# Kernel tuning notes

Hardware: AMD Instinct MI355X
Metric: run time of the kernel (lower is better)

Reference implementation:

```python
import jax, jax.numpy as jnp
import numpy as np

N = 100000

def _gcn_layer(x, W, b, row, col, n):
    # x: [N, Fin] -> lin -> [N, Fout]
    h = x @ W + b
    # degree over row (includes self loops), dtype follows x
    deg = jnp.zeros((n,), dtype=h.dtype).at[row].add(jnp.ones_like(row, dtype=h.dtype))
    dis = deg ** -0.5
    norm = dis[row] * dis[col]                      # [E]
    msg = norm[:, None] * h[row]                    # gather + scale: [E, Fout]
    return jax.ops.segment_sum(msg, col, num_segments=n)  # scatter-add at targets


def setup_inputs() -> dict:
    key = jax.random.key(0)
    ks = jax.random.split(key, 10)
    x = jax.random.normal(ks[0], (N, 32), dtype=jnp.float32)
    feat = jax.random.normal(ks[1], (N, 32), dtype=jnp.float32)
    edge_index = jax.random.randint(ks[2], (2, 1600000), 0, N, dtype=jnp.int64)
    # params (torch Linear stored as [in, out] here; y = x @ W + b)
    def lin(k, fin, fout):
        s = 1.0 / np.sqrt(fin)
        kw, kb = jax.random.split(k)
        W = jax.random.uniform(kw, (fin, fout), minval=-s, maxval=s, dtype=jnp.float32)
        b = jax.random.uniform(kb, (fout,), minval=-s, maxval=s, dtype=jnp.float32)
        return W, b
    W1, b1 = lin(ks[3], 64, 64)
    W2, b2 = lin(ks[4], 64, 64)
    Wfc, bfc = lin(ks[5], 64, 64)
    return {"x": x, "feat": feat, "edge_index": edge_index,
            "W1": W1, "b1": b1, "W2": W2, "b2": b2, "Wfc": Wfc, "bfc": bfc}


def reference(x, feat, edge_index, W1, b1, W2, b2, Wfc, bfc):
    n = x.shape[0]
    h = jnp.concatenate([x, feat], axis=-1)          # [N, 64]
    # add self loops once (same augmented edge set used by every layer)
    loops = jnp.arange(n, dtype=edge_index.dtype)
    row = jnp.concatenate([edge_index[0], loops])
    col = jnp.concatenate([edge_index[1], loops])
    h = jax.nn.relu(_gcn_layer(h, W1, b1, row, col, n))
    h = jax.nn.relu(_gcn_layer(h, W2, b2, row, col, n))
    return jax.nn.relu(h @ Wfc + bfc)                # [N, 64]
```

## Files before the change

### kernel.cpp

```cpp
#include <hip/hip_runtime.h>
#include <hip/hip_bf16.h>


#define FDIM 64
#define NPART 8
#define GPB 64
#define NB 256
#define BW 512
#define MAXP 1024
#define GPLIN 1024

typedef __hip_bfloat16 bf16;
typedef short v8s __attribute__((ext_vector_type(8)));
typedef float v4f __attribute__((ext_vector_type(4)));

__global__ void k_h(const int* __restrict__ row, const int* __restrict__ col,
                    unsigned* __restrict__ part, int* __restrict__ M,
                    int E, int n, int psize, int P, int CH) {
    __shared__ unsigned sm[12512];
    int t = threadIdx.x, b = blockIdx.x;
    if (b < NPART * GPB) {
        int p = b >> 6, g = b & 63;
        int base = p * psize;
        int lim = n - base; if (lim > psize) lim = psize;
        for (int i = t; i < lim; i += 256) sm[i] = 0u;
        __syncthreads();
        for (int e = g * 256 + t; e < E; e += GPB * 256) {
            int r = row[e] - base;
            if ((unsigned)r < (unsigned)lim) atomicAdd(&sm[r], 1u);
        }
        __syncthreads();
        unsigned* dst = part + ((size_t)p * GPB + g) * psize;
        for (int i = t; i < lim; i += 256) dst[i] = sm[i];
    } else {
        int cb = b - NPART * GPB;
        int* h = (int*)sm;
        for (int i = t; i < P; i += 256) h[i] = 0;
        __syncthreads();
        int s = cb * CH, e = min(s + CH, E);
        for (int i = s + t; i < e; i += 256)
            atomicAdd(&h[col[i] >> 9], 1);
        __syncthreads();
        for (int p = t; p < P; p += 256) M[p * NB + cb] = h[p];
    }
}

__global__ void k_ds1(const unsigned* __restrict__ part, float* __restrict__ dis,
                      int* __restrict__ M, int* __restrict__ bsum,
                      int n, int psize, int ndis, int P) {
    __shared__ int sc[256];
    int t = threadIdx.x, b = blockIdx.x;
    if (b < ndis) {
        int i = b * 256 + t;
        if (i >= n) return;
        int p = i / psize, loc = i - p * psize;
        const unsigned* src = part + (size_t)p * GPB * psize + loc;
        unsigned s = 0;
        #pragma unroll 8
        for (int g = 0; g < GPB; ++g) s += src[(size_t)g * psize];
        dis[i] = rsqrtf((float)s + 1.0f);
    } else {
        int sb = b - ndis;
        int i = sb * 256 + t;
        int v = M[i];
        sc[t] = v;
        __syncthreads();
        for (int d = 1; d < 256; d <<= 1) {
            int u = (t >= d) ? sc[t - d] : 0;
            __syncthreads(); sc[t] += u; __syncthreads();
        }
        M[i] = sc[t] - v;
        if (t == 255) bsum[sb] = sc[255];
    }
}

__global__ void k_csc(const int* __restrict__ row, const int* __restrict__ col,
                      const int* __restrict__ M, const int* __restrict__ bsum,
                      int* __restrict__ s4, int E, int CH, int P) {
    __shared__ int sc[256];
    __shared__ int bs[256];
    __shared__ int cur[MAXP];
    int t = threadIdx.x, b = blockIdx.x;
    int v = (t < P) ? bsum[t] : 0;
    sc[t] = v;
    __syncthreads();
    for (int d = 1; d < 256; d <<= 1) {
        int u = (t >= d) ? sc[t - d] : 0;
        __syncthreads(); sc[t] += u; __syncthreads();
    }
    bs[t] = sc[t] - v;
    __syncthreads();
    for (int p = t; p < P; p += 256) cur[p] = bs[p] + M[p * NB + b];
    __syncthreads();
    int s = b * CH, e = min(s + CH, E);
    for (int i = s + t; i < e; i += 256) {
        int r = row[i], c = col[i];
        int pos = atomicAdd(&cur[c >> 9], 1);
        s4[pos] = (r << 9) | (c & 511);
    }
}

__global__ __launch_bounds__(256, 4)
void k_fl(const int* __restrict__ s4, const int* __restrict__ M,
          const int* __restrict__ bsum, int* __restrict__ rows4,
          int* __restrict__ off,
          const float* __restrict__ x, const float* __restrict__ feat,
          const float* __restrict__ W, const float* __restrict__ bvec,
          const float* __restrict__ dis, bf16* __restrict__ g1,
          int n, int E, int P) {
    __shared__ int sc[256];
    __shared__ int bs[256];
    __shared__ int hist[BW];
    __shared__ int loff[BW];
    __shared__ int tmp[256];
    __shared__ float sIn[4][FDIM];
    int t = threadIdx.x, b = blockIdx.x;
    if (b < P) {
        int v = (t < P) ? bsum[t] : 0;
        sc[t] = v;
        __syncthreads();
        for (int d = 1; d < 256; d <<= 1) {
            int u = (t >= d) ? sc[t - d] : 0;
            __syncthreads(); sc[t] += u; __syncthreads();
        }
        bs[t] = sc[t] - v;
        __syncthreads();
        int gs = bs[b];
        int ge = gs + bsum[b];
        int c0 = b << 9;
        int lim = n - c0; if (lim > BW) lim = BW;
        hist[2 * t] = 0; hist[2 * t + 1] = 0;
        __syncthreads();
        for (int i = gs + t; i < ge; i += 256)
            atomicAdd(&hist[s4[i] & 511], 1);
        __syncthreads();
        int s0 = hist[2 * t], s1v = hist[2 * t + 1];
        int ps = s0 + s1v;
        tmp[t] = ps;
        __syncthreads();
        for (int d = 1; d < 256; d <<= 1) {
            int u = (t >= d) ? tmp[t - d] : 0;
            __syncthreads(); tmp[t] += u; __syncthreads();
        }
        int ex = tmp[t] - ps;
        loff[2 * t] = ex;
        loff[2 * t + 1] = ex + s0;
        __syncthreads();
        for (int i = t; i < lim; i += 256) off[c0 + i] = gs + loff[i];
        if (b == P - 1 && t == 0) off[n] = E;
        __syncthreads();
        for (int i = gs + t; i < ge; i += 256) {
            int v2 = s4[i];
            int pos = gs + atomicAdd(&loff[v2 & 511], 1);
            rows4[pos] = v2 >> 9;
        }
    } else {
        int local = t >> 6, j = t & 63;
        float Wreg[FDIM];
        #pragma unroll
        for (int k = 0; k < FDIM; ++k) Wreg[k] = W[k * FDIM + j];
        float bj = bvec[j];
        int gw = (b - P) * 4 + local;
        int nwl = GPLIN * 4;
        for (int w = gw; w < n; w += nwl) {
            sIn[local][j] = (j < 32) ? x[(size_t)w * 32 + j]
                                     : feat[(size_t)w * 32 + (j - 32)];
            __threadfence_block();
            float o = bj;
            #pragma unroll
            for (int k4 = 0; k4 < 16; ++k4) {
                float4 h4 = *(const float4*)&sIn[local][k4 * 4];
                o = fmaf(h4.x, Wreg[4 * k4 + 0], o);
                o = fmaf(h4.y, Wreg[4 * k4 + 1], o);
                o = fmaf(h4.z, Wreg[4 * k4 + 2], o);
                o = fmaf(h4.w, Wreg[4 * k4 + 3], o);
            }
            g1[(size_t)w * FDIM + j] = __float2bfloat16(dis[w] * o);
            __threadfence_block();
        }
    }
}

__global__ __launch_bounds__(256, 8)
void k_gather(const int* __restrict__ rows4, const int* __restrict__ off,
              const float* __restrict__ dis, const bf16* __restrict__ g,
              bf16* __restrict__ a, int n) {
    int t = blockIdx.x * blockDim.x + threadIdx.x;
    int w = t >> 6, j = t & 63;
    if (w >= n) return;
    float acc0 = __bfloat162float(g[(size_t)w * FDIM + j]);
    float acc1 = 0.0f;
    int k = off[w], e = off[w + 1];
    for (; k + 8 <= e; k += 8) {
        int r0 = rows4[k], r1 = rows4[k + 1], r2 = rows4[k + 2], r3 = rows4[k + 3];
        int r4 = rows4[k + 4], r5 = rows4[k + 5], r6 = rows4[k + 6], r7 = rows4[k + 7];
        float h0 = __bfloat162float(g[(size_t)r0 * FDIM + j]);
        float h1 = __bfloat162float(g[(size_t)r1 * FDIM + j]);
        float h2 = __bfloat162float(g[(size_t)r2 * FDIM + j]);
        float h3 = __bfloat162float(g[(size_t)r3 * FDIM + j]);
        float h4 = __bfloat162float(g[(size_t)r4 * FDIM + j]);
        float h5 = __bfloat162float(g[(size_t)r5 * FDIM + j]);
        float h6 = __bfloat162float(g[(size_t)r6 * FDIM + j]);
        float h7 = __bfloat162float(g[(size_t)r7 * FDIM + j]);
        acc0 += h0; acc1 += h1; acc0 += h2; acc1 += h3;
        acc0 += h4; acc1 += h5; acc0 += h6; acc1 += h7;
    }
    for (; k + 2 <= e; k += 2) {
        int r0 = rows4[k], r1 = rows4[k + 1];
        acc0 += __bfloat162float(g[(size_t)r0 * FDIM + j]);
        acc1 += __bfloat162float(g[(size_t)r1 * FDIM + j]);
    }
    if (k < e) acc0 += __bfloat162float(g[(size_t)rows4[k] * FDIM + j]);
    a[(size_t)w * FDIM + j] = __float2bfloat16(fmaxf(dis[w] * (acc0 + acc1), 0.0f));
}

template <bool FINAL>
__global__ __launch_bounds__(256, 4)
void k_mat(const bf16* __restrict__ A, const float* __restrict__ W,
           const float* __restrict__ bvec, const float* __restrict__ dis,
           void* __restrict__ outp, int n) {
    __shared__ __align__(16) bf16 sWt[FDIM * FDIM];
    int t = threadIdx.x;
    for (int idx = t; idx < FDIM * FDIM; idx += 256) {
        int kk = idx >> 6, nn = idx & 63;
        sWt[nn * FDIM + kk] = __float2bfloat16(W[idx]);
    }
    __syncthreads();
    int wave = t >> 6, lane = t & 63;
    int quad = lane >> 4, l15 = lane & 15;
    v8s bfr[4][2];
    #pragma unroll
    for (int nt = 0; nt < 4; ++nt) {
        #pragma unroll
        for (int kf = 0; kf < 2; ++kf)
            bfr[nt][kf] = *(const v8s*)&sWt[(nt * 16 + l15) * FDIM + kf * 32 + quad * 8];
    }
    float bj[4];
    #pragma unroll
    for (int nt = 0; nt < 4; ++nt) bj[nt] = bvec[nt * 16 + l15];

    int ntiles = (n + 15) >> 4;
    int step = gridDim.x * 4;
    for (int tile = blockIdx.x * 4 + wave; tile < ntiles; tile += step) {
        int m0 = tile << 4;
        int mA = m0 + l15; if (mA >= n) mA = n - 1;
        v8s af0 = *(const v8s*)&A[(size_t)mA * FDIM + quad * 8];
        v8s af1 = *(const v8s*)&A[(size_t)mA * FDIM + 32 + quad * 8];
        v4f acc[4];
        #pragma unroll
        for (int nt = 0; nt < 4; ++nt) {
            acc[nt] = (v4f){0.f, 0.f, 0.f, 0.f};
            acc[nt] = __builtin_amdgcn_mfma_f32_16x16x32_bf16(af0, bfr[nt][0], acc[nt], 0, 0, 0);
            acc[nt] = __builtin_amdgcn_mfma_f32_16x16x32_bf16(af1, bfr[nt][1], acc[nt], 0, 0, 0);
        }
        #pragma unroll
        for (int r = 0; r < 4; ++r) {
            int node = m0 + quad * 4 + r;
            if (node >= n) continue;
            float dv = FINAL ? 0.0f : dis[node];
            #pragma unroll
            for (int nt = 0; nt < 4; ++nt) {
                int j = nt * 16 + l15;
                float o = acc[nt][r] + bj[nt];
                if (FINAL) ((float*)outp)[(size_t)node * FDIM + j] = fmaxf(o, 0.0f);
                else ((bf16*)outp)[(size_t)node * FDIM + j] = __float2bfloat16(dv * o);
            }
        }
    }
}

extern "C" void kernel_launch(void* const* d_in, const int* in_sizes, int n_in,
                              void* d_out, int out_size, void* d_ws, size_t ws_size,
                              hipStream_t stream) {
    const float* x    = (const float*)d_in[0];
    const float* feat = (const float*)d_in[1];
    const int*   ei   = (const int*)d_in[2];
    const float* W1   = (const float*)d_in[3];
    const float* b1   = (const float*)d_in[4];
    const float* W2   = (const float*)d_in[5];
    const float* b2   = (const float*)d_in[6];
    const float* Wfc  = (const float*)d_in[7];
    const float* bfc  = (const float*)d_in[8];
    float* out = (float*)d_out;

    const int n = in_sizes[0] / 32;
    const int E = in_sizes[2] / 2;
    const int* row = ei;
    const int* col = ei + E;

    const int psize = (n + NPART - 1) / NPART;
    const int P  = (n + BW - 1) / BW;
    const int CH = (E + NB - 1) / NB;
    const int total = P * NB;
    const int ndis = (n + 255) / 256;

    int*   off  = (int*)d_ws;
    float* dis  = (float*)(off + (size_t)n + 1);
    int*   M    = (int*)(dis + n);
    int*   bsum = M + (size_t)total;
    int*   s4    = bsum + 256;
    int*   rows4 = s4 + E;
    size_t co = (size_t)(rows4 + E - (int*)d_ws);
    co = (co + 3) & ~(size_t)3;
    bf16*  bufA  = (bf16*)((int*)d_ws + co);
    bf16*  bufB  = bufA + (size_t)n * FDIM;
    unsigned* part = (unsigned*)bufA;

    const int B = 256;

    k_h<<<NPART * GPB + NB, B, 0, stream>>>(row, col, part, M, E, n, psize, P, CH);
    k_ds1<<<ndis + P, B, 0, stream>>>(part, dis, M, bsum, n, psize, ndis, P);
    k_csc<<<NB, B, 0, stream>>>(row, col, M, bsum, s4, E, CH, P);
    k_fl<<<P + GPLIN, B, 0, stream>>>(s4, M, bsum, rows4, off,
                                      x, feat, W1, b1, dis, bufA, n, E, P);
    k_gather<<<(n + 3) / 4, B, 0, stream>>>(rows4, off, dis, bufA, bufB, n);
    k_mat<false><<<512, B, 0, stream>>>(bufB, W2, b2, dis, bufA, n);
    k_gather<<<(n + 3) / 4, B, 0, stream>>>(rows4, off, dis, bufA, bufB, n);
    k_mat<true><<<512, B, 0, stream>>>(bufB, Wfc, bfc, dis, out, n);
}
```

Before: 315.0 us.

## Split features into two 32-wide slabs and gather with 16-byte vector loads

Stores the intermediate bf16 feature matrices as two column slabs of 32 features each, so each row in a slab is 64 bytes. The gather kernel runs one pass per slab, with each wave handling 16 edges at once: four lanes per edge, each loading 8 bf16 values as one vector. It then reduces across lanes with shuffles. This replaces the old scheme, where each lane read one 2-byte element per edge, and is meant to improve memory-level parallelism and cache-line use for the random row gathers. The cost is shuffle reductions, wasted lanes on low-degree nodes, and twice as many gather blocks.

```diff
diff --git a/kernel.cpp b/kernel.cpp
--- a/kernel.cpp
+++ b/kernel.cpp
@@ -13,6 +13,16 @@
 typedef __hip_bfloat16 bf16;
 typedef short v8s __attribute__((ext_vector_type(8)));
 typedef float v4f __attribute__((ext_vector_type(4)));
+
+static __device__ __forceinline__ float b2f(short s) {
+    union { unsigned u; float f; } v;
+    v.u = ((unsigned)(unsigned short)s) << 16;
+    return v.f;
+}
+static __device__ __forceinline__ short f2b(float f) {
+    bf16 b = __float2bfloat16(f);
+    return *(short*)&b;
+}
 
 __global__ void k_h(const int* __restrict__ row, const int* __restrict__ col,
                     unsigned* __restrict__ part, int* __restrict__ M,
@@ -162,6 +172,7 @@
         float bj = bvec[j];
         int gw = (b - P) * 4 + local;
         int nwl = GPLIN * 4;
+        int slab = j >> 5, jo = j & 31;
         for (int w = gw; w < n; w += nwl) {
             sIn[local][j] = (j < 32) ? x[(size_t)w * 32 + j]
                                      : feat[(size_t)w * 32 + (j - 32)];
@@ -175,7 +186,8 @@
                 o = fmaf(h4.z, Wreg[4 * k4 + 2], o);
                 o = fmaf(h4.w, Wreg[4 * k4 + 3], o);
             }
-            g1[(size_t)w * FDIM + j] = __float2bfloat16(dis[w] * o);
+            g1[(size_t)slab * n * 32 + (size_t)w * 32 + jo] =
+                __float2bfloat16(dis[w] * o);
             __threadfence_block();
         }
     }
@@ -184,34 +196,42 @@
 __global__ __launch_bounds__(256, 8)
 void k_gather(const int* __restrict__ rows4, const int* __restrict__ off,
               const float* __restrict__ dis, const bf16* __restrict__ g,
-              bf16* __restrict__ a, int n) {
-    int t = blockIdx.x * blockDim.x + threadIdx.x;
-    int w = t >> 6, j = t & 63;
-    if (w >= n) return;
-    float acc0 = __bfloat162float(g[(size_t)w * FDIM + j]);
-    float acc1 = 0.0f;
-    int k = off[w], e = off[w + 1];
-    for (; k + 8 <= e; k += 8) {
-        int r0 = rows4[k], r1 = rows4[k + 1], r2 = rows4[k + 2], r3 = rows4[k + 3];
-        int r4 = rows4[k + 4], r5 = rows4[k + 5], r6 = rows4[k + 6], r7 = rows4[k + 7];
-        float h0 = __bfloat162float(g[(size_t)r0 * FDIM + j]);
-        float h1 = __bfloat162float(g[(size_t)r1 * FDIM + j]);
-        float h2 = __bfloat162float(g[(size_t)r2 * FDIM + j]);
-        float h3 = __bfloat162float(g[(size_t)r3 * FDIM + j]);
-        float h4 = __bfloat162float(g[(size_t)r4 * FDIM + j]);
-        float h5 = __bfloat162float(g[(size_t)r5 * FDIM + j]);
-        float h6 = __bfloat162float(g[(size_t)r6 * FDIM + j]);
-        float h7 = __bfloat162float(g[(size_t)r7 * FDIM + j]);
-        acc0 += h0; acc1 += h1; acc0 += h2; acc1 += h3;
-        acc0 += h4; acc1 += h5; acc0 += h6; acc1 += h7;
-    }
-    for (; k + 2 <= e; k += 2) {
-        int r0 = rows4[k], r1 = rows4[k + 1];
-        acc0 += __bfloat162float(g[(size_t)r0 * FDIM + j]);
-        acc1 += __bfloat162float(g[(size_t)r1 * FDIM + j]);
-    }
-    if (k < e) acc0 += __bfloat162float(g[(size_t)rows4[k] * FDIM + j]);
-    a[(size_t)w * FDIM + j] = __float2bfloat16(fmaxf(dis[w] * (acc0 + acc1), 0.0f));
+              bf16* __restrict__ a, int n, int nb0) {
+    int b = blockIdx.x;
+    int pass = (b >= nb0) ? 1 : 0;
+    int wv = (b - pass * nb0) * 4 + (threadIdx.x >> 6);
+    if (wv >= n) return;
+    int lane = threadIdx.x & 63;
+    int fq = lane & 3;
+    int es = lane >> 2;
+    const bf16* gs = g + (size_t)pass * n * 32;
+    bf16* as = a + (size_t)pass * n * 32;
+    float acc[8];
+    #pragma unroll
+    for (int q = 0; q < 8; ++q) acc[q] = 0.0f;
+    int s = off[wv], e = off[wv + 1];
+    for (int k = s; k < e; k += 16) {
+        int idx = k + es;
+        int r = __builtin_nontemporal_load(rows4 + min(idx, e - 1));
+        v8s hv = *(const v8s*)&gs[(size_t)r * 32 + fq * 8];
+        float wgt = (idx < e) ? 1.0f : 0.0f;
+        #pragma unroll
+        for (int q = 0; q < 8; ++q) acc[q] = fmaf(wgt, b2f(hv[q]), acc[q]);
+    }
+    #pragma unroll
+    for (int m = 4; m <= 32; m <<= 1) {
+        #pragma unroll
+        for (int q = 0; q < 8; ++q) acc[q] += __shfl_xor(acc[q], m, 64);
+    }
+    if (es == 0) {
+        v8s sv = *(const v8s*)&gs[(size_t)wv * 32 + fq * 8];
+        float dv = dis[wv];
+        v8s ov;
+        #pragma unroll
+        for (int q = 0; q < 8; ++q)
+            ov[q] = f2b(fmaxf(dv * (acc[q] + b2f(sv[q])), 0.0f));
+        __builtin_nontemporal_store(ov, (v8s*)&as[(size_t)wv * 32 + fq * 8]);
+    }
 }
 
 template <bool FINAL>
@@ -239,13 +259,16 @@
     #pragma unroll
     for (int nt = 0; nt < 4; ++nt) bj[nt] = bvec[nt * 16 + l15];
 
+    const bf16* Alo = A;
+    const bf16* Ahi = A + (size_t)n * 32;
+
     int ntiles = (n + 15) >> 4;
     int step = gridDim.x * 4;
     for (int tile = blockIdx.x * 4 + wave; tile < ntiles; tile += step) {
         int m0 = tile << 4;
         int mA = m0 + l15; if (mA >= n) mA = n - 1;
-        v8s af0 = *(const v8s*)&A[(size_t)mA * FDIM + quad * 8];
-        v8s af1 = *(const v8s*)&A[(size_t)mA * FDIM + 32 + quad * 8];
+        v8s af0 = *(const v8s*)&Alo[(size_t)mA * 32 + quad * 8];
+        v8s af1 = *(const v8s*)&Ahi[(size_t)mA * 32 + quad * 8];
         v4f acc[4];
         #pragma unroll
         for (int nt = 0; nt < 4; ++nt) {
@@ -262,8 +285,12 @@
             for (int nt = 0; nt < 4; ++nt) {
                 int j = nt * 16 + l15;
                 float o = acc[nt][r] + bj[nt];
-                if (FINAL) ((float*)outp)[(size_t)node * FDIM + j] = fmaxf(o, 0.0f);
-                else ((bf16*)outp)[(size_t)node * FDIM + j] = __float2bfloat16(dv * o);
+                if (FINAL) {
+                    ((float*)outp)[(size_t)node * FDIM + j] = fmaxf(o, 0.0f);
+                } else {
+                    ((bf16*)outp)[(size_t)(j >> 5) * n * 32 + (size_t)node * 32 + (j & 31)] =
+                        __float2bfloat16(dv * o);
+                }
             }
         }
     }
@@ -307,14 +334,15 @@
     unsigned* part = (unsigned*)bufA;
 
     const int B = 256;
+    const int nb0 = (n + 3) / 4;
 
     k_h<<<NPART * GPB + NB, B, 0, stream>>>(row, col, part, M, E, n, psize, P, CH);
     k_ds1<<<ndis + P, B, 0, stream>>>(part, dis, M, bsum, n, psize, ndis, P);
     k_csc<<<NB, B, 0, stream>>>(row, col, M, bsum, s4, E, CH, P);
     k_fl<<<P + GPLIN, B, 0, stream>>>(s4, M, bsum, rows4, off,
                                       x, feat, W1, b1, dis, bufA, n, E, P);
-    k_gather<<<(n + 3) / 4, B, 0, stream>>>(rows4, off, dis, bufA, bufB, n);
+    k_gather<<<2 * nb0, B, 0, stream>>>(rows4, off, dis, bufA, bufB, n, nb0);
     k_mat<false><<<512, B, 0, stream>>>(bufB, W2, b2, dis, bufA, n);
-    k_gather<<<(n + 3) / 4, B, 0, stream>>>(rows4, off, dis, bufA, bufB, n);
+    k_gather<<<2 * nb0, B, 0, stream>>>(rows4, off, dis, bufA, bufB, n, nb0);
     k_mat<true><<<512, B, 0, stream>>>(bufB, Wfc, bfc, dis, out, n);
 }
```

Result: slower. 369.4 us (+17.3%).
